# Kernel optimization log

Measured on AMD Instinct MI355X. Metric: run time of the kernel, lower is better.

The kernel has to match this reference:

```python
import jax, jax.numpy as jnp
import numpy as np

NEG_SLOPE = 0.01  # torch nn.LeakyReLU default
B, C, H, W = 2, 128, 192, 192
K = 4            # num_cls
O = 12 * 5       # out_channels = 12 * num_mix


def _lrelu(x):
    return jnp.where(x >= 0, x, NEG_SLOPE * x)


def _conv1x1(x, w, b):
    # x: [B,K,C,H,W] (or [B,C,H,W] broadcast via K in w), w: [K,O,C], b: [K,O]
    y = jnp.einsum('bkchw,koc->bkohw', x, w)
    return y + b[None, :, :, None, None]


def setup_inputs() -> dict:
    key = jax.random.key(0)
    ks = jax.random.split(key, 12)
    s = 1.0 / np.sqrt(C)
    inp = {
        'fusion_context': jax.random.normal(ks[0], (B, C, H, W), jnp.float32),
        'seg': jax.random.randint(ks[1], (B, 1, H, W), 0, K, jnp.int64),
        'W1':  jax.random.normal(ks[2], (K, C, C), jnp.float32) * s,
        'b1':  jax.random.normal(ks[3], (K, C), jnp.float32) * s,
        'Wr1': jax.random.normal(ks[4], (K, C, C), jnp.float32) * s,
        'br1': jax.random.normal(ks[5], (K, C), jnp.float32) * s,
        'Wr2': jax.random.normal(ks[6], (K, C, C), jnp.float32) * s,
        'br2': jax.random.normal(ks[7], (K, C), jnp.float32) * s,
        'W3':  jax.random.normal(ks[8], (K, C, C), jnp.float32) * s,
        'b3':  jax.random.normal(ks[9], (K, C), jnp.float32) * s,
        'W4':  jax.random.normal(ks[10], (K, O, C), jnp.float32) * s,
        'b4':  jax.random.normal(ks[11], (K, O), jnp.float32) * s,
    }
    return inp


def reference(fusion_context, seg, W1, b1, Wr1, br1, Wr2, br2, W3, b3, W4, b4):
    x = fusion_context[:, None]                      # [B,1,C,H,W] -> broadcast over K towers
    x = jnp.broadcast_to(x, (B, K, C, H, W))
    h = _conv1x1(x, W1, b1)                          # conv1x1(ep_ch, ep_ch)
    # ResBlock_1x1: x + conv(lrelu(conv(x)))
    r = _conv1x1(_lrelu(_conv1x1(h, Wr1, br1)), Wr2, br2)
    h = h + r
    h = _conv1x1(h, W3, b3)                          # conv1x1(ep_ch, ep_ch)
    h = _lrelu(h)                                    # LeakyReLU
    conv_outs = _conv1x1(h, W4, b4)                  # [B,K,O,H,W]
    # one-hot mask-and-sum over classes
    seg2 = seg[:, 0]                                 # [B,H,W]
    one_hot = jax.nn.one_hot(seg2, K, dtype=conv_outs.dtype)  # [B,H,W,K]
    one_hot = jnp.transpose(one_hot, (0, 3, 1, 2))   # [B,K,H,W]
    out = jnp.sum(conv_outs * one_hot[:, :, None], axis=1)    # [B,O,H,W]
    return out
```

## Files before the change

### kernel.cpp

```cpp
#include <hip/hip_runtime.h>
#include <hip/hip_bf16.h>
#include <cstdint>
#include <cstddef>

constexpr int kB = 2, kC = 128, kH = 192, kW = 192, kK = 4, kO = 60;
constexpr int kHW  = kH * kW;
constexpr int NPIX = kB * kHW;
constexpr int P    = 96;
constexpr int WPB  = kHW / P;
constexpr int NWIN = NPIX / P;
constexpr int MAXG = 9;
constexpr float kSlope = 0.01f;

constexpr size_t WB_OFF    = 0;
constexpr size_t WB4_OFF   = 524288;
constexpr size_t BIAS_OFF  = 589824;
constexpr size_t BIAS4_OFF = 598016;
constexpr size_t WS_NEED   = 599040;

typedef __attribute__((ext_vector_type(8))) short bf16x8;
typedef __attribute__((ext_vector_type(4))) float f32x4;

__device__ __forceinline__ unsigned short f2bf(float f) {
  unsigned u = __float_as_uint(f);
  u += 0x7FFF + ((u >> 16) & 1);
  return (unsigned short)(u >> 16);
}
__device__ __forceinline__ float bf2f(unsigned short u) {
  return __uint_as_float(((unsigned)u) << 16);
}
__device__ __forceinline__ float load1(const float* p) { return *p; }
__device__ __forceinline__ float load1(const __hip_bfloat16* p) {
  return bf2f(*reinterpret_cast<const unsigned short*>(p));
}
__device__ __forceinline__ bf16x8 load_wfrag(const __hip_bfloat16* p) {
  return *reinterpret_cast<const bf16x8*>(p);
}
__device__ __forceinline__ bf16x8 load_wfrag(const float* p) {
  bf16x8 r;
#pragma unroll
  for (int j = 0; j < 8; ++j) r[j] = (short)f2bf(p[j]);
  return r;
}

__device__ __forceinline__ int xgrp(int r, int g) {
  return (g + r + (r >> 3)) & 15;
}

struct alignas(16) Smem {
  unsigned short Xs[P][kC];
  unsigned short Ys[P][kC];
  short ord[MAXG * 16];
  unsigned char kg[MAXG + 3];
  int cnt[kK], gpre[kK + 1], first[kK];
  int s_f32, s_onz;
};

template<typename T>
__device__ __forceinline__ void prep_body(
    const T* W1, const T* Wr1, const T* Wr2, const T* W3, const T* W4,
    const T* b1, const T* br1, const T* br2, const T* b3, const T* b4,
    char* ws, int gid) {
  unsigned short* WB  = (unsigned short*)(ws + WB_OFF);
  unsigned short* WB4 = (unsigned short*)(ws + WB4_OFF);
  float* BS  = (float*)(ws + BIAS_OFF);
  float* BS4 = (float*)(ws + BIAS4_OFF);
  if (gid < 32768) {
    const int lk = gid >> 11, fl = gid & 2047, f = fl >> 6, lane = fl & 63;
    const int l = lk >> 2, k = lk & 3;
    const int rb = f >> 3, oi = (f >> 2) & 1, ks = f & 3;
    const int quad = lane >> 4, col = lane & 15;
    const int row = rb * 32 + oi * 16 + col, c0 = ks * 32 + quad * 8;
    const T* Wsrc = (l == 0) ? W1 : (l == 1) ? Wr1 : (l == 2) ? Wr2 : W3;
    bf16x8 v = load_wfrag(Wsrc + ((size_t)(k * kC + row)) * kC + c0);
    *reinterpret_cast<bf16x8*>(WB + (size_t)lk * 16384 + f * 512 + lane * 8) = v;
  } else if (gid < 36864) {
    const int g2 = gid - 32768, k = g2 >> 10, fl = g2 & 1023, f = fl >> 6, lane = fl & 63;
    const int rb = f >> 2, ks = f & 3, quad = lane >> 4, col = lane & 15;
    const int row = rb * 16 + col, c0 = ks * 32 + quad * 8;
    bf16x8 v;
    if (row < kO) v = load_wfrag(W4 + ((size_t)(k * kO + row)) * kC + c0);
    else { for (int j = 0; j < 8; ++j) v[j] = 0; }
    *reinterpret_cast<bf16x8*>(WB4 + (size_t)k * 8192 + f * 512 + lane * 8) = v;
  } else if (gid < 38912) {
    const int g2 = gid - 36864, l = g2 >> 9, kn = g2 & 511, k = kn >> 7, n = kn & 127;
    const T* bsrc = (l == 0) ? b1 : (l == 1) ? br1 : (l == 2) ? br2 : b3;
    BS[g2] = load1(bsrc + k * kC + n);
  } else if (gid < 39168) {
    const int g2 = gid - 38912, k = g2 >> 6, n = g2 & 63;
    BS4[g2] = (n < kO) ? load1(b4 + k * kO + n) : 0.f;
  }
}

__global__ __launch_bounds__(256) void prep_kernel(
    const void* W1, const void* Wr1, const void* Wr2, const void* W3, const void* W4,
    const void* b1, const void* br1, const void* br2, const void* b3, const void* b4,
    char* ws) {
  __shared__ int s_f32;
  if (threadIdx.x == 0) s_f32 = 0;
  __syncthreads();
  const unsigned short h = ((const unsigned short*)W1)[threadIdx.x];
  if (((h >> 7) & 0xFF) >= 0x84) atomicAdd(&s_f32, 1);
  __syncthreads();
  const int gid = blockIdx.x * 256 + threadIdx.x;
  if (s_f32 > 8)
    prep_body<float>((const float*)W1, (const float*)Wr1, (const float*)Wr2,
                     (const float*)W3, (const float*)W4, (const float*)b1,
                     (const float*)br1, (const float*)br2, (const float*)b3,
                     (const float*)b4, ws, gid);
  else
    prep_body<__hip_bfloat16>((const __hip_bfloat16*)W1, (const __hip_bfloat16*)Wr1,
                              (const __hip_bfloat16*)Wr2, (const __hip_bfloat16*)W3,
                              (const __hip_bfloat16*)W4, (const __hip_bfloat16*)b1,
                              (const __hip_bfloat16*)br1, (const __hip_bfloat16*)br2,
                              (const __hip_bfloat16*)b3, (const __hip_bfloat16*)b4,
                              ws, gid);
}

template<bool SNIFFX>
__device__ __forceinline__ void prologue(const void* xraw, const void* segraw,
                                         Smem& sm, int bb, int hw0, int tid) {
  if (tid == 0) { sm.s_f32 = 0; sm.s_onz = 0; }
  if (tid < kK) sm.cnt[tid] = 0;
  __syncthreads();
  if constexpr (SNIFFX) {
    const unsigned short h = ((const unsigned short*)xraw)[tid];
    if (((h >> 7) & 0xFF) >= 0x84) atomicAdd(&sm.s_f32, 1);
  }
  if (tid < 288 && (tid & 1) && ((const unsigned*)segraw)[tid] != 0)
    atomicAdd(&sm.s_onz, 1);
  __syncthreads();
  const bool is64 = (sm.s_onz < 4);
  int myk = 0, myidx = 0;
  if (tid < P) {
    const int pg = bb * kHW + hw0 + tid;
    myk = is64 ? (int)((const long long*)segraw)[pg]
               : ((const int*)segraw)[pg];
    myidx = atomicAdd(&sm.cnt[myk], 1);
    if (myidx == 0) sm.first[myk] = tid;
  }
  __syncthreads();
  if (tid == 0) {
    int g = 0;
    for (int k = 0; k < kK; ++k) {
      sm.gpre[k] = g;
      const int gc = (sm.cnt[k] + 15) >> 4;
      for (int j = 0; j < gc; ++j) sm.kg[g + j] = (unsigned char)k;
      g += gc;
    }
    sm.gpre[kK] = g;
  }
  __syncthreads();
  if (tid < P) sm.ord[sm.gpre[myk] * 16 + myidx] = (short)tid;
  const int ngrp = sm.gpre[kK];
  if (tid < ngrp * 16) {
    const int g = tid >> 4, k2 = sm.kg[g];
    const int rel = tid - sm.gpre[k2] * 16;
    if (rel >= sm.cnt[k2])
      sm.ord[tid] = (short)(sm.first[k2] | 256);
  }
}

template<typename T>
__device__ __forceinline__ void stage(const void* xraw, unsigned short (*Xs)[kC],
                                      int bb, int hw0, int tid) {
  const T* x = (const T*)xraw;
  const size_t base = (size_t)bb * kC * kHW + hw0;
  if constexpr (sizeof(T) == 4) {
#pragma unroll
    for (int it = 0; it < 6; ++it) {
      const int flat = it * 512 + tid;
      const int c = flat / 24, j = flat - c * 24;
      const float4 v = *reinterpret_cast<const float4*>(
          (const float*)x + base + (size_t)c * kHW + j * 4);
      const float vv[4] = {v.x, v.y, v.z, v.w};
#pragma unroll
      for (int jj = 0; jj < 4; ++jj) {
        const int r = j * 4 + jj;
        Xs[r][xgrp(r, c >> 3) * 8 + (c & 7)] = f2bf(vv[jj]);
      }
    }
  } else {
#pragma unroll
    for (int it = 0; it < 3; ++it) {
      const int flat = it * 512 + tid;
      const int c = flat / 12, j = flat - c * 12;
      const bf16x8 v = *reinterpret_cast<const bf16x8*>(
          (const unsigned short*)x + base + (size_t)c * kHW + j * 8);
#pragma unroll
      for (int jj = 0; jj < 8; ++jj) {
        const int r = j * 8 + jj;
        Xs[r][xgrp(r, c >> 3) * 8 + (c & 7)] = (unsigned short)v[jj];
      }
    }
  }
}

template<typename T>
__device__ __forceinline__ void output(void* outraw, const float* Obuf,
                                       int bb, int hw0, int tid) {
  T* ob = (T*)outraw + (size_t)bb * kO * kHW + hw0;
  if constexpr (sizeof(T) == 4) {
#pragma unroll
    for (int it = 0; it < 3; ++it) {
      const int t = it * 512 + tid;
      if (t < 1440) {
        const int o = t / 24, q = t - o * 24;
        float4 v;
        v.x = Obuf[(q * 4 + 0) * 61 + o];
        v.y = Obuf[(q * 4 + 1) * 61 + o];
        v.z = Obuf[(q * 4 + 2) * 61 + o];
        v.w = Obuf[(q * 4 + 3) * 61 + o];
        *reinterpret_cast<float4*>((float*)ob + (size_t)o * kHW + q * 4) = v;
      }
    }
  } else {
#pragma unroll
    for (int it = 0; it < 6; ++it) {
      const int t = it * 512 + tid;
      if (t < 2880) {
        const int o = t / 48, q = t - o * 48;
        const unsigned u = (unsigned)f2bf(Obuf[(q * 2) * 61 + o]) |
                           ((unsigned)f2bf(Obuf[(q * 2 + 1) * 61 + o]) << 16);
        *reinterpret_cast<unsigned*>((unsigned short*)ob + (size_t)o * kHW + q * 2) = u;
      }
    }
  }
}

template<bool LRELU, bool RES, bool PAIR>
__device__ __forceinline__ void pair_body(const unsigned short (*src)[kC],
                                          unsigned short (*dst)[kC],
                                          const bf16x8 (&a)[2][4],
                                          const float4 (&bv)[2],
                                          const Smem& sm, int g,
                                          int quad, int col, int rb) {
  constexpr int NG = PAIR ? 2 : 1;
  int ov[2], row[2];
  bf16x8 bfr[2][4];
#pragma unroll
  for (int j = 0; j < NG; ++j) {
    ov[j]  = sm.ord[(g + j) * 16 + col];
    row[j] = ov[j] & 255;
#pragma unroll
    for (int ks = 0; ks < 4; ++ks)
      bfr[j][ks] = *reinterpret_cast<const bf16x8*>(
          &src[row[j]][xgrp(row[j], ks * 4 + quad) * 8]);
  }
  f32x4 acc[2][2];
#pragma unroll
  for (int j = 0; j < NG; ++j)
#pragma unroll
    for (int oi = 0; oi < 2; ++oi) {
      acc[j][oi] = {0.f, 0.f, 0.f, 0.f};
#pragma unroll
      for (int ks = 0; ks < 4; ++ks)
        acc[j][oi] = __builtin_amdgcn_mfma_f32_16x16x32_bf16(
            a[oi][ks], bfr[j][ks], acc[j][oi], 0, 0, 0);
    }
#pragma unroll
  for (int j = 0; j < NG; ++j) {
    if (ov[j] < 256) {
#pragma unroll
      for (int oi = 0; oi < 2; ++oi) {
        const int nb = rb * 32 + oi * 16 + quad * 4;
        unsigned short* dp = &dst[row[j]][xgrp(row[j], nb >> 3) * 8 + (nb & 7)];
        const float bb4[4] = {bv[oi].x, bv[oi].y, bv[oi].z, bv[oi].w};
        float v[4];
#pragma unroll
        for (int r = 0; r < 4; ++r) {
          float t = acc[j][oi][r] + bb4[r];
          if constexpr (LRELU) t = (t >= 0.f) ? t : kSlope * t;
          v[r] = t;
        }
        if constexpr (RES) {
          const short4 rv = *reinterpret_cast<const short4*>(dp);
          v[0] += bf2f((unsigned short)rv.x);
          v[1] += bf2f((unsigned short)rv.y);
          v[2] += bf2f((unsigned short)rv.z);
          v[3] += bf2f((unsigned short)rv.w);
        }
        short4 pk;
        pk.x = (short)f2bf(v[0]); pk.y = (short)f2bf(v[1]);
        pk.z = (short)f2bf(v[2]); pk.w = (short)f2bf(v[3]);
        *reinterpret_cast<short4*>(dp) = pk;
      }
    }
  }
}

template<bool LRELU, bool RES>
__device__ __forceinline__ void layerP(const unsigned short (*src)[kC],
                                       unsigned short (*dst)[kC],
                                       const unsigned short* __restrict__ WBl,
                                       const float* __restrict__ BSl,
                                       const Smem& sm, int tid) {
  const int wave = tid >> 6, lane = tid & 63, quad = lane >> 4, col = lane & 15;
  const int rb = wave & 3, ch2 = wave >> 2;
#pragma unroll
  for (int c2 = 0; c2 < 2; ++c2) {
    const int k = ch2 * 2 + c2;
    const int gs = sm.gpre[k], ge = sm.gpre[k + 1];
    if (gs == ge) continue;
    const unsigned short* wk = WBl + (size_t)k * 16384 + lane * 8;
    bf16x8 a[2][4];
    float4 bv[2];
#pragma unroll
    for (int oi = 0; oi < 2; ++oi) {
#pragma unroll
      for (int ks = 0; ks < 4; ++ks)
        a[oi][ks] = *reinterpret_cast<const bf16x8*>(wk + (((rb * 2 + oi) * 4 + ks) << 9));
      bv[oi] = *reinterpret_cast<const float4*>(
          BSl + k * kC + rb * 32 + oi * 16 + quad * 4);
    }
    int g = gs;
    for (; g + 1 < ge; g += 2)
      pair_body<LRELU, RES, true >(src, dst, a, bv, sm, g, quad, col, rb);
    if (g < ge)
      pair_body<LRELU, RES, false>(src, dst, a, bv, sm, g, quad, col, rb);
  }
}

template<bool PAIR>
__device__ __forceinline__ void pair_body5(const unsigned short (*src)[kC],
                                           float* __restrict__ Obuf,
                                           const bf16x8 (&a)[4],
                                           const float4& bv,
                                           const Smem& sm, int g,
                                           int quad, int col, int rb) {
  constexpr int NG = PAIR ? 2 : 1;
  int ov[2], row[2];
  bf16x8 bfr[2][4];
#pragma unroll
  for (int j = 0; j < NG; ++j) {
    ov[j]  = sm.ord[(g + j) * 16 + col];
    row[j] = ov[j] & 255;
#pragma unroll
    for (int ks = 0; ks < 4; ++ks)
      bfr[j][ks] = *reinterpret_cast<const bf16x8*>(
          &src[row[j]][xgrp(row[j], ks * 4 + quad) * 8]);
  }
  f32x4 acc[2];
#pragma unroll
  for (int j = 0; j < NG; ++j) {
    acc[j] = {0.f, 0.f, 0.f, 0.f};
#pragma unroll
    for (int ks = 0; ks < 4; ++ks)
      acc[j] = __builtin_amdgcn_mfma_f32_16x16x32_bf16(a[ks], bfr[j][ks], acc[j], 0, 0, 0);
  }
  const float bb4[4] = {bv.x, bv.y, bv.z, bv.w};
#pragma unroll
  for (int j = 0; j < NG; ++j) {
    if (ov[j] < 256) {
#pragma unroll
      for (int r = 0; r < 4; ++r) {
        const int n = rb * 16 + quad * 4 + r;
        if (n < kO) Obuf[row[j] * 61 + n] = acc[j][r] + bb4[r];
      }
    }
  }
}

__device__ __forceinline__ void layer5P(const unsigned short (*src)[kC],
                                        float* __restrict__ Obuf,
                                        const unsigned short* __restrict__ WB4,
                                        const float* __restrict__ BS4,
                                        const Smem& sm, int tid) {
  const int wave = tid >> 6, lane = tid & 63, quad = lane >> 4, col = lane & 15;
  const int rb = wave & 3, ch2 = wave >> 2;
#pragma unroll
  for (int c2 = 0; c2 < 2; ++c2) {
    const int k = ch2 * 2 + c2;
    const int gs = sm.gpre[k], ge = sm.gpre[k + 1];
    if (gs == ge) continue;
    const unsigned short* wk = WB4 + (size_t)k * 8192 + lane * 8;
    bf16x8 a[4];
#pragma unroll
    for (int ks = 0; ks < 4; ++ks)
      a[ks] = *reinterpret_cast<const bf16x8*>(wk + ((rb * 4 + ks) << 9));
    const float4 bv = *reinterpret_cast<const float4*>(
        BS4 + k * 64 + rb * 16 + quad * 4);
    int g = gs;
    for (; g + 1 < ge; g += 2)
      pair_body5<true >(src, Obuf, a, bv, sm, g, quad, col, rb);
    if (g < ge)
      pair_body5<false>(src, Obuf, a, bv, sm, g, quad, col, rb);
  }
}

__global__ __launch_bounds__(512, 4) void fused_main(const void* xraw, const void* segraw,
                                                     void* outraw,
                                                     const char* __restrict__ ws) {
  __shared__ Smem sm;
  const int tid = threadIdx.x, wi = blockIdx.x;
  const int bb = wi / WPB, hw0 = (wi - bb * WPB) * P;
  prologue<true>(xraw, segraw, sm, bb, hw0, tid);
  const bool isf32 = (sm.s_f32 > 16);
  if (isf32) stage<float>(xraw, sm.Xs, bb, hw0, tid);
  else       stage<__hip_bfloat16>(xraw, sm.Xs, bb, hw0, tid);
  __syncthreads();

  const unsigned short* WB  = (const unsigned short*)(ws + WB_OFF);
  const unsigned short* WB4 = (const unsigned short*)(ws + WB4_OFF);
  const float* BS  = (const float*)(ws + BIAS_OFF);
  const float* BS4 = (const float*)(ws + BIAS4_OFF);

  layerP<false, false>(sm.Xs, sm.Ys, WB,              BS,        sm, tid); __syncthreads();
  layerP<true,  false>(sm.Ys, sm.Xs, WB + 4 * 16384,  BS + 512,  sm, tid); __syncthreads();
  layerP<false, true >(sm.Xs, sm.Ys, WB + 8 * 16384,  BS + 1024, sm, tid); __syncthreads();
  layerP<true,  false>(sm.Ys, sm.Xs, WB + 12 * 16384, BS + 1536, sm, tid); __syncthreads();
  float* Obuf = (float*)sm.Ys;
  layer5P(sm.Xs, Obuf, WB4, BS4, sm, tid);     __syncthreads();

  if (isf32) output<float>(outraw, Obuf, bb, hw0, tid);
  else       output<__hip_bfloat16>(outraw, Obuf, bb, hw0, tid);
}

template<typename T, bool LRELU, bool RES>
__device__ __forceinline__ void layerF(const unsigned short (*src)[kC],
                                       unsigned short (*dst)[kC],
                                       const T* __restrict__ W,
                                       const T* __restrict__ bia,
                                       const Smem& sm, int tid) {
  const int wave = tid >> 6, lane = tid & 63, quad = lane >> 4, col = lane & 15;
  const int rb = wave & 3, ch2 = wave >> 2;
  const int gs = sm.gpre[ch2 * 2], ge = sm.gpre[ch2 * 2 + 2];
  int curk = -1;
  bf16x8 a[2][4];
  float bs[2][4];
  for (int g = gs; g < ge; ++g) {
    const int k = sm.kg[g];
    if (k != curk) {
      curk = k;
      const T* Wk = W + (size_t)k * kC * kC;
      const T* bk = bia + (size_t)k * kC;
#pragma unroll
      for (int oi = 0; oi < 2; ++oi) {
        const int ra = rb * 32 + oi * 16 + col;
#pragma unroll
        for (int ks = 0; ks < 4; ++ks)
          a[oi][ks] = load_wfrag(Wk + (size_t)ra * kC + ks * 32 + quad * 8);
#pragma unroll
        for (int r = 0; r < 4; ++r)
          bs[oi][r] = load1(bk + rb * 32 + oi * 16 + quad * 4 + r);
      }
    }
    const int ov  = sm.ord[g * 16 + col];
    const int row = ov & 255;
    bf16x8 bfr[4];
#pragma unroll
    for (int ks = 0; ks < 4; ++ks)
      bfr[ks] = *reinterpret_cast<const bf16x8*>(&src[row][xgrp(row, ks * 4 + quad) * 8]);
#pragma unroll
    for (int oi = 0; oi < 2; ++oi) {
      f32x4 acc = {0.f, 0.f, 0.f, 0.f};
#pragma unroll
      for (int ks = 0; ks < 4; ++ks)
        acc = __builtin_amdgcn_mfma_f32_16x16x32_bf16(a[oi][ks], bfr[ks], acc, 0, 0, 0);
      if (ov < 256) {
        const int nb = rb * 32 + oi * 16 + quad * 4;
        unsigned short* dp = &dst[row][xgrp(row, nb >> 3) * 8 + (nb & 7)];
        float v[4];
#pragma unroll
        for (int r = 0; r < 4; ++r) {
          float t = acc[r] + bs[oi][r];
          if constexpr (LRELU) t = (t >= 0.f) ? t : kSlope * t;
          v[r] = t;
        }
        if constexpr (RES) {
          const short4 rv = *reinterpret_cast<const short4*>(dp);
          v[0] += bf2f((unsigned short)rv.x);
          v[1] += bf2f((unsigned short)rv.y);
          v[2] += bf2f((unsigned short)rv.z);
          v[3] += bf2f((unsigned short)rv.w);
        }
        short4 pk;
        pk.x = (short)f2bf(v[0]); pk.y = (short)f2bf(v[1]);
        pk.z = (short)f2bf(v[2]); pk.w = (short)f2bf(v[3]);
        *reinterpret_cast<short4*>(dp) = pk;
      }
    }
  }
}

template<typename T>
__device__ __forceinline__ void layer5F(const unsigned short (*src)[kC],
                                        float* __restrict__ Obuf,
                                        const T* __restrict__ W4,
                                        const T* __restrict__ b4,
                                        const Smem& sm, int tid) {
  const int wave = tid >> 6, lane = tid & 63, quad = lane >> 4, col = lane & 15;
  const int rb = wave & 3, ch2 = wave >> 2;
  const int gs = sm.gpre[ch2 * 2], ge = sm.gpre[ch2 * 2 + 2];
  int curk = -1;
  bf16x8 a[4];
  float bs[4];
  for (int g = gs; g < ge; ++g) {
    const int k = sm.kg[g];
    if (k != curk) {
      curk = k;
      const T* Wk = W4 + (size_t)k * kO * kC;
      const T* bk = b4 + (size_t)k * kO;
      const int ra = min(rb * 16 + col, kO - 1);
#pragma unroll
      for (int ks = 0; ks < 4; ++ks)
        a[ks] = load_wfrag(Wk + (size_t)ra * kC + ks * 32 + quad * 8);
#pragma unroll
      for (int r = 0; r < 4; ++r) {
        const int n = rb * 16 + quad * 4 + r;
        bs[r] = (n < kO) ? load1(bk + n) : 0.f;
      }
    }
    const int ov  = sm.ord[g * 16 + col];
    const int row = ov & 255;
    bf16x8 bfr[4];
#pragma unroll
    for (int ks = 0; ks < 4; ++ks)
      bfr[ks] = *reinterpret_cast<const bf16x8*>(&src[row][xgrp(row, ks * 4 + quad) * 8]);
    f32x4 acc = {0.f, 0.f, 0.f, 0.f};
#pragma unroll
    for (int ks = 0; ks < 4; ++ks)
      acc = __builtin_amdgcn_mfma_f32_16x16x32_bf16(a[ks], bfr[ks], acc, 0, 0, 0);
    if (ov < 256) {
#pragma unroll
      for (int r = 0; r < 4; ++r) {
        const int n = rb * 16 + quad * 4 + r;
        if (n < kO) Obuf[row * 61 + n] = acc[r] + bs[r];
      }
    }
  }
}

template<typename T>
__device__ __forceinline__ void run_fall(
    const void* xraw, void* outraw,
    const void* W1, const void* b1, const void* Wr1, const void* br1,
    const void* Wr2, const void* br2, const void* W3, const void* b3,
    const void* W4, const void* b4,
    Smem& sm, int bb, int hw0, int tid) {
  stage<T>(xraw, sm.Xs, bb, hw0, tid);
  __syncthreads();
  layerF<T, false, false>(sm.Xs, sm.Ys, (const T*)W1,  (const T*)b1,  sm, tid); __syncthreads();
  layerF<T, true,  false>(sm.Ys, sm.Xs, (const T*)Wr1, (const T*)br1, sm, tid); __syncthreads();
  layerF<T, false, true >(sm.Xs, sm.Ys, (const T*)Wr2, (const T*)br2, sm, tid); __syncthreads();
  layerF<T, true,  false>(sm.Ys, sm.Xs, (const T*)W3,  (const T*)b3,  sm, tid); __syncthreads();
  float* Obuf = (float*)sm.Ys;
  layer5F<T>(sm.Xs, Obuf, (const T*)W4, (const T*)b4, sm, tid);
  __syncthreads();
  output<T>(outraw, Obuf, bb, hw0, tid);
}

__global__ __launch_bounds__(512) void fused_fallback(
    const void* xraw, const void* segraw,
    const void* W1, const void* b1, const void* Wr1, const void* br1,
    const void* Wr2, const void* br2, const void* W3, const void* b3,
    const void* W4, const void* b4, void* outraw) {
  __shared__ Smem sm;
  const int tid = threadIdx.x, wi = blockIdx.x;
  const int bb = wi / WPB, hw0 = (wi - bb * WPB) * P;
  prologue<true>(xraw, segraw, sm, bb, hw0, tid);
  if (sm.s_f32 > 16)
    run_fall<float>(xraw, outraw, W1, b1, Wr1, br1, Wr2, br2, W3, b3, W4, b4,
                    sm, bb, hw0, tid);
  else
    run_fall<__hip_bfloat16>(xraw, outraw, W1, b1, Wr1, br1, Wr2, br2, W3, b3, W4, b4,
                             sm, bb, hw0, tid);
}

extern "C" void kernel_launch(void* const* d_in, const int* in_sizes, int n_in,
                              void* d_out, int out_size, void* d_ws, size_t ws_size,
                              hipStream_t stream) {
  (void)in_sizes; (void)n_in; (void)out_size;
  const int prep = (d_ws != nullptr && ws_size >= WS_NEED) ? 1 : 0;
  if (prep) {
    prep_kernel<<<153, 256, 0, stream>>>(
        d_in[2], d_in[4], d_in[6], d_in[8], d_in[10],
        d_in[3], d_in[5], d_in[7], d_in[9], d_in[11], (char*)d_ws);
    fused_main<<<NWIN, 512, 0, stream>>>(d_in[0], d_in[1], d_out, (const char*)d_ws);
  } else {
    fused_fallback<<<NWIN, 512, 0, stream>>>(
        d_in[0], d_in[1], d_in[2], d_in[3], d_in[4], d_in[5], d_in[6], d_in[7],
        d_in[8], d_in[9], d_in[10], d_in[11], d_out);
  }
}
```

Baseline: 130.1 us.

## Interleave class groups across wave halves and store intermediates in class-compacted order

Measured after the change: 141.3 us. 8.5% more time.

```diff
diff --git a/kernel.cpp b/kernel.cpp
--- a/kernel.cpp
+++ b/kernel.cpp
@@ -52,6 +52,8 @@
   unsigned short Ys[P][kC];
   short ord[MAXG * 16];
   unsigned char kg[MAXG + 3];
+  unsigned char gb[MAXG + 3];
+  unsigned char gv[MAXG + 3];
   int cnt[kK], gpre[kK + 1], first[kK];
   int s_f32, s_onz;
 };
@@ -141,12 +143,17 @@
   }
   __syncthreads();
   if (tid == 0) {
-    int g = 0;
+    int g = 0, cb = 0;
     for (int k = 0; k < kK; ++k) {
       sm.gpre[k] = g;
       const int gc = (sm.cnt[k] + 15) >> 4;
-      for (int j = 0; j < gc; ++j) sm.kg[g + j] = (unsigned char)k;
+      for (int j = 0; j < gc; ++j) {
+        sm.kg[g + j] = (unsigned char)k;
+        sm.gb[g + j] = (unsigned char)(cb + j * 16);
+        sm.gv[g + j] = (unsigned char)min(16, sm.cnt[k] - j * 16);
+      }
       g += gc;
+      cb += sm.cnt[k];
     }
     sm.gpre[kK] = g;
   }
@@ -228,24 +235,34 @@
   }
 }
 
-template<bool LRELU, bool RES, bool PAIR>
+template<bool LRELU, bool RES, bool PAIR, bool SRCPIX>
 __device__ __forceinline__ void pair_body(const unsigned short (*src)[kC],
                                           unsigned short (*dst)[kC],
                                           const bf16x8 (&a)[2][4],
                                           const float4 (&bv)[2],
-                                          const Smem& sm, int g,
+                                          const Smem& sm, int g0, int g1,
                                           int quad, int col, int rb) {
   constexpr int NG = PAIR ? 2 : 1;
-  int ov[2], row[2];
+  const int gg[2] = {g0, g1};
+  int srow[2], drow[2];
+  bool valid[2];
   bf16x8 bfr[2][4];
 #pragma unroll
   for (int j = 0; j < NG; ++j) {
-    ov[j]  = sm.ord[(g + j) * 16 + col];
-    row[j] = ov[j] & 255;
+    const int g = gg[j];
+    const int vc = sm.gv[g];
+    const int base = sm.gb[g];
+    drow[j]  = base + col;
+    valid[j] = (col < vc);
+    if constexpr (SRCPIX) {
+      srow[j] = sm.ord[g * 16 + col] & 255;
+    } else {
+      srow[j] = base + min(col, vc - 1);
+    }
 #pragma unroll
     for (int ks = 0; ks < 4; ++ks)
       bfr[j][ks] = *reinterpret_cast<const bf16x8*>(
-          &src[row[j]][xgrp(row[j], ks * 4 + quad) * 8]);
+          &src[srow[j]][xgrp(srow[j], ks * 4 + quad) * 8]);
   }
   f32x4 acc[2][2];
 #pragma unroll
@@ -260,11 +277,11 @@
     }
 #pragma unroll
   for (int j = 0; j < NG; ++j) {
-    if (ov[j] < 256) {
+    if (valid[j]) {
 #pragma unroll
       for (int oi = 0; oi < 2; ++oi) {
         const int nb = rb * 32 + oi * 16 + quad * 4;
-        unsigned short* dp = &dst[row[j]][xgrp(row[j], nb >> 3) * 8 + (nb & 7)];
+        unsigned short* dp = &dst[drow[j]][xgrp(drow[j], nb >> 3) * 8 + (nb & 7)];
         const float bb4[4] = {bv[oi].x, bv[oi].y, bv[oi].z, bv[oi].w};
         float v[4];
 #pragma unroll
@@ -289,35 +306,40 @@
   }
 }
 
-template<bool LRELU, bool RES>
+template<bool LRELU, bool RES, bool SRCPIX>
 __device__ __forceinline__ void layerP(const unsigned short (*src)[kC],
                                        unsigned short (*dst)[kC],
                                        const unsigned short* __restrict__ WBl,
                                        const float* __restrict__ BSl,
                                        const Smem& sm, int tid) {
   const int wave = tid >> 6, lane = tid & 63, quad = lane >> 4, col = lane & 15;
-  const int rb = wave & 3, ch2 = wave >> 2;
-#pragma unroll
-  for (int c2 = 0; c2 < 2; ++c2) {
-    const int k = ch2 * 2 + c2;
-    const int gs = sm.gpre[k], ge = sm.gpre[k + 1];
-    if (gs == ge) continue;
-    const unsigned short* wk = WBl + (size_t)k * 16384 + lane * 8;
-    bf16x8 a[2][4];
-    float4 bv[2];
-#pragma unroll
-    for (int oi = 0; oi < 2; ++oi) {
-#pragma unroll
-      for (int ks = 0; ks < 4; ++ks)
-        a[oi][ks] = *reinterpret_cast<const bf16x8*>(wk + (((rb * 2 + oi) * 4 + ks) << 9));
-      bv[oi] = *reinterpret_cast<const float4*>(
-          BSl + k * kC + rb * 32 + oi * 16 + quad * 4);
-    }
-    int g = gs;
-    for (; g + 1 < ge; g += 2)
-      pair_body<LRELU, RES, true >(src, dst, a, bv, sm, g, quad, col, rb);
-    if (g < ge)
-      pair_body<LRELU, RES, false>(src, dst, a, bv, sm, g, quad, col, rb);
+  const int rb = wave & 3, half = wave >> 2;
+  const int ngrp = sm.gpre[kK];
+  int curk = -1;
+  bf16x8 a[2][4];
+  float4 bv[2];
+  int g = half;
+  while (g < ngrp) {
+    const int k = sm.kg[g];
+    if (k != curk) {
+      curk = k;
+      const unsigned short* wk = WBl + (size_t)k * 16384 + lane * 8;
+#pragma unroll
+      for (int oi = 0; oi < 2; ++oi) {
+#pragma unroll
+        for (int ks = 0; ks < 4; ++ks)
+          a[oi][ks] = *reinterpret_cast<const bf16x8*>(wk + (((rb * 2 + oi) * 4 + ks) << 9));
+        bv[oi] = *reinterpret_cast<const float4*>(
+            BSl + k * kC + rb * 32 + oi * 16 + quad * 4);
+      }
+    }
+    if (g + 2 < ngrp && sm.kg[g + 2] == k) {
+      pair_body<LRELU, RES, true, SRCPIX>(src, dst, a, bv, sm, g, g + 2, quad, col, rb);
+      g += 4;
+    } else {
+      pair_body<LRELU, RES, false, SRCPIX>(src, dst, a, bv, sm, g, g, quad, col, rb);
+      g += 2;
+    }
   }
 }
 
@@ -326,19 +348,24 @@
                                            float* __restrict__ Obuf,
                                            const bf16x8 (&a)[4],
                                            const float4& bv,
-                                           const Smem& sm, int g,
+                                           const Smem& sm, int g0, int g1,
                                            int quad, int col, int rb) {
   constexpr int NG = PAIR ? 2 : 1;
-  int ov[2], row[2];
+  const int gg[2] = {g0, g1};
+  int srow[2], pix[2];
+  bool valid[2];
   bf16x8 bfr[2][4];
 #pragma unroll
   for (int j = 0; j < NG; ++j) {
-    ov[j]  = sm.ord[(g + j) * 16 + col];
-    row[j] = ov[j] & 255;
+    const int g = gg[j];
+    const int vc = sm.gv[g];
+    srow[j]  = sm.gb[g] + min(col, vc - 1);
+    valid[j] = (col < vc);
+    pix[j]   = sm.ord[g * 16 + col] & 255;
 #pragma unroll
     for (int ks = 0; ks < 4; ++ks)
       bfr[j][ks] = *reinterpret_cast<const bf16x8*>(
-          &src[row[j]][xgrp(row[j], ks * 4 + quad) * 8]);
+          &src[srow[j]][xgrp(srow[j], ks * 4 + quad) * 8]);
   }
   f32x4 acc[2];
 #pragma unroll
@@ -351,11 +378,11 @@
   const float bb4[4] = {bv.x, bv.y, bv.z, bv.w};
 #pragma unroll
   for (int j = 0; j < NG; ++j) {
-    if (ov[j] < 256) {
+    if (valid[j]) {
 #pragma unroll
       for (int r = 0; r < 4; ++r) {
         const int n = rb * 16 + quad * 4 + r;
-        if (n < kO) Obuf[row[j] * 61 + n] = acc[j][r] + bb4[r];
+        if (n < kO) Obuf[pix[j] * 61 + n] = acc[j][r] + bb4[r];
       }
     }
   }
@@ -367,24 +394,29 @@
                                         const float* __restrict__ BS4,
                                         const Smem& sm, int tid) {
   const int wave = tid >> 6, lane = tid & 63, quad = lane >> 4, col = lane & 15;
-  const int rb = wave & 3, ch2 = wave >> 2;
-#pragma unroll
-  for (int c2 = 0; c2 < 2; ++c2) {
-    const int k = ch2 * 2 + c2;
-    const int gs = sm.gpre[k], ge = sm.gpre[k + 1];
-    if (gs == ge) continue;
-    const unsigned short* wk = WB4 + (size_t)k * 8192 + lane * 8;
-    bf16x8 a[4];
-#pragma unroll
-    for (int ks = 0; ks < 4; ++ks)
-      a[ks] = *reinterpret_cast<const bf16x8*>(wk + ((rb * 4 + ks) << 9));
-    const float4 bv = *reinterpret_cast<const float4*>(
-        BS4 + k * 64 + rb * 16 + quad * 4);
-    int g = gs;
-    for (; g + 1 < ge; g += 2)
-      pair_body5<true >(src, Obuf, a, bv, sm, g, quad, col, rb);
-    if (g < ge)
-      pair_body5<false>(src, Obuf, a, bv, sm, g, quad, col, rb);
+  const int rb = wave & 3, half = wave >> 2;
+  const int ngrp = sm.gpre[kK];
+  int curk = -1;
+  bf16x8 a[4];
+  float4 bv;
+  int g = half;
+  while (g < ngrp) {
+    const int k = sm.kg[g];
+    if (k != curk) {
+      curk = k;
+      const unsigned short* wk = WB4 + (size_t)k * 8192 + lane * 8;
+#pragma unroll
+      for (int ks = 0; ks < 4; ++ks)
+        a[ks] = *reinterpret_cast<const bf16x8*>(wk + ((rb * 4 + ks) << 9));
+      bv = *reinterpret_cast<const float4*>(BS4 + k * 64 + rb * 16 + quad * 4);
+    }
+    if (g + 2 < ngrp && sm.kg[g + 2] == k) {
+      pair_body5<true >(src, Obuf, a, bv, sm, g, g + 2, quad, col, rb);
+      g += 4;
+    } else {
+      pair_body5<false>(src, Obuf, a, bv, sm, g, g, quad, col, rb);
+      g += 2;
+    }
   }
 }
 
@@ -405,10 +437,10 @@
   const float* BS  = (const float*)(ws + BIAS_OFF);
   const float* BS4 = (const float*)(ws + BIAS4_OFF);
 
-  layerP<false, false>(sm.Xs, sm.Ys, WB,              BS,        sm, tid); __syncthreads();
-  layerP<true,  false>(sm.Ys, sm.Xs, WB + 4 * 16384,  BS + 512,  sm, tid); __syncthreads();
-  layerP<false, true >(sm.Xs, sm.Ys, WB + 8 * 16384,  BS + 1024, sm, tid); __syncthreads();
-  layerP<true,  false>(sm.Ys, sm.Xs, WB + 12 * 16384, BS + 1536, sm, tid); __syncthreads();
+  layerP<false, false, true >(sm.Xs, sm.Ys, WB,              BS,        sm, tid); __syncthreads();
+  layerP<true,  false, false>(sm.Ys, sm.Xs, WB + 4 * 16384,  BS + 512,  sm, tid); __syncthreads();
+  layerP<false, true,  false>(sm.Xs, sm.Ys, WB + 8 * 16384,  BS + 1024, sm, tid); __syncthreads();
+  layerP<true,  false, false>(sm.Ys, sm.Xs, WB + 12 * 16384, BS + 1536, sm, tid); __syncthreads();
   float* Obuf = (float*)sm.Ys;
   layer5P(sm.Xs, Obuf, WB4, BS4, sm, tid);     __syncthreads();
 
```

## Store intermediate activations in class-sorted compact rows and fold bias into MFMA accumulator

Applied to the files above, without the earlier changes.

Result: slower. 133.4 us (+2.5%).

```diff
diff --git a/kernel.cpp b/kernel.cpp
--- a/kernel.cpp
+++ b/kernel.cpp
@@ -29,6 +29,12 @@
 __device__ __forceinline__ float bf2f(unsigned short u) {
   return __uint_as_float(((unsigned)u) << 16);
 }
+__device__ __forceinline__ unsigned pack2bf(float lo, float hi) {
+  float2 f2; f2.x = lo; f2.y = hi;
+  __hip_bfloat162 h = __float22bfloat162_rn(f2);
+  unsigned u; __builtin_memcpy(&u, &h, sizeof(u));
+  return u;
+}
 __device__ __forceinline__ float load1(const float* p) { return *p; }
 __device__ __forceinline__ float load1(const __hip_bfloat16* p) {
   return bf2f(*reinterpret_cast<const unsigned short*>(p));
@@ -52,6 +58,8 @@
   unsigned short Ys[P][kC];
   short ord[MAXG * 16];
   unsigned char kg[MAXG + 3];
+  unsigned char gb[MAXG + 3];
+  unsigned char gv[MAXG + 3];
   int cnt[kK], gpre[kK + 1], first[kK];
   int s_f32, s_onz;
 };
@@ -141,12 +149,17 @@
   }
   __syncthreads();
   if (tid == 0) {
-    int g = 0;
+    int g = 0, cb = 0;
     for (int k = 0; k < kK; ++k) {
       sm.gpre[k] = g;
       const int gc = (sm.cnt[k] + 15) >> 4;
-      for (int j = 0; j < gc; ++j) sm.kg[g + j] = (unsigned char)k;
+      for (int j = 0; j < gc; ++j) {
+        sm.kg[g + j] = (unsigned char)k;
+        sm.gb[g + j] = (unsigned char)(cb + j * 16);
+        sm.gv[g + j] = (unsigned char)min(16, sm.cnt[k] - j * 16);
+      }
       g += gc;
+      cb += sm.cnt[k];
     }
     sm.gpre[kK] = g;
   }
@@ -220,39 +233,44 @@
       const int t = it * 512 + tid;
       if (t < 2880) {
         const int o = t / 48, q = t - o * 48;
-        const unsigned u = (unsigned)f2bf(Obuf[(q * 2) * 61 + o]) |
-                           ((unsigned)f2bf(Obuf[(q * 2 + 1) * 61 + o]) << 16);
+        const unsigned u = pack2bf(Obuf[(q * 2) * 61 + o], Obuf[(q * 2 + 1) * 61 + o]);
         *reinterpret_cast<unsigned*>((unsigned short*)ob + (size_t)o * kHW + q * 2) = u;
       }
     }
   }
 }
 
-template<bool LRELU, bool RES, bool PAIR>
+template<bool LRELU, bool RES, bool PAIR, bool SRCPIX>
 __device__ __forceinline__ void pair_body(const unsigned short (*src)[kC],
                                           unsigned short (*dst)[kC],
                                           const bf16x8 (&a)[2][4],
-                                          const float4 (&bv)[2],
-                                          const Smem& sm, int g,
+                                          const f32x4 (&bv)[2],
+                                          const Smem& sm, int g0,
                                           int quad, int col, int rb) {
   constexpr int NG = PAIR ? 2 : 1;
-  int ov[2], row[2];
+  int srow[2], drow[2];
+  bool valid[2];
   bf16x8 bfr[2][4];
 #pragma unroll
   for (int j = 0; j < NG; ++j) {
-    ov[j]  = sm.ord[(g + j) * 16 + col];
-    row[j] = ov[j] & 255;
+    const int g = g0 + j;
+    const int vc = sm.gv[g];
+    const int base = sm.gb[g];
+    drow[j]  = base + col;
+    valid[j] = (col < vc);
+    if constexpr (SRCPIX) srow[j] = sm.ord[g * 16 + col] & 255;
+    else                  srow[j] = base + min(col, vc - 1);
 #pragma unroll
     for (int ks = 0; ks < 4; ++ks)
       bfr[j][ks] = *reinterpret_cast<const bf16x8*>(
-          &src[row[j]][xgrp(row[j], ks * 4 + quad) * 8]);
+          &src[srow[j]][xgrp(srow[j], ks * 4 + quad) * 8]);
   }
   f32x4 acc[2][2];
 #pragma unroll
   for (int j = 0; j < NG; ++j)
 #pragma unroll
     for (int oi = 0; oi < 2; ++oi) {
-      acc[j][oi] = {0.f, 0.f, 0.f, 0.f};
+      acc[j][oi] = bv[oi];
 #pragma unroll
       for (int ks = 0; ks < 4; ++ks)
         acc[j][oi] = __builtin_amdgcn_mfma_f32_16x16x32_bf16(
@@ -260,36 +278,35 @@
     }
 #pragma unroll
   for (int j = 0; j < NG; ++j) {
-    if (ov[j] < 256) {
+    if (valid[j]) {
 #pragma unroll
       for (int oi = 0; oi < 2; ++oi) {
         const int nb = rb * 32 + oi * 16 + quad * 4;
-        unsigned short* dp = &dst[row[j]][xgrp(row[j], nb >> 3) * 8 + (nb & 7)];
-        const float bb4[4] = {bv[oi].x, bv[oi].y, bv[oi].z, bv[oi].w};
+        unsigned short* dp = &dst[drow[j]][xgrp(drow[j], nb >> 3) * 8 + (nb & 7)];
         float v[4];
 #pragma unroll
         for (int r = 0; r < 4; ++r) {
-          float t = acc[j][oi][r] + bb4[r];
+          float t = acc[j][oi][r];
           if constexpr (LRELU) t = (t >= 0.f) ? t : kSlope * t;
           v[r] = t;
         }
         if constexpr (RES) {
-          const short4 rv = *reinterpret_cast<const short4*>(dp);
-          v[0] += bf2f((unsigned short)rv.x);
-          v[1] += bf2f((unsigned short)rv.y);
-          v[2] += bf2f((unsigned short)rv.z);
-          v[3] += bf2f((unsigned short)rv.w);
+          const uint2 rv = *reinterpret_cast<const uint2*>(dp);
+          v[0] += bf2f((unsigned short)(rv.x & 0xFFFFu));
+          v[1] += bf2f((unsigned short)(rv.x >> 16));
+          v[2] += bf2f((unsigned short)(rv.y & 0xFFFFu));
+          v[3] += bf2f((unsigned short)(rv.y >> 16));
         }
-        short4 pk;
-        pk.x = (short)f2bf(v[0]); pk.y = (short)f2bf(v[1]);
-        pk.z = (short)f2bf(v[2]); pk.w = (short)f2bf(v[3]);
-        *reinterpret_cast<short4*>(dp) = pk;
-      }
-    }
-  }
-}
-
-template<bool LRELU, bool RES>
+        uint2 pk;
+        pk.x = pack2bf(v[0], v[1]);
+        pk.y = pack2bf(v[2], v[3]);
+        *reinterpret_cast<uint2*>(dp) = pk;
+      }
+    }
+  }
+}
+
+template<bool LRELU, bool RES, bool SRCPIX>
 __device__ __forceinline__ void layerP(const unsigned short (*src)[kC],
                                        unsigned short (*dst)[kC],
                                        const unsigned short* __restrict__ WBl,
@@ -304,20 +321,21 @@
     if (gs == ge) continue;
     const unsigned short* wk = WBl + (size_t)k * 16384 + lane * 8;
     bf16x8 a[2][4];
-    float4 bv[2];
+    f32x4 bv[2];
 #pragma unroll
     for (int oi = 0; oi < 2; ++oi) {
 #pragma unroll
       for (int ks = 0; ks < 4; ++ks)
         a[oi][ks] = *reinterpret_cast<const bf16x8*>(wk + (((rb * 2 + oi) * 4 + ks) << 9));
-      bv[oi] = *reinterpret_cast<const float4*>(
+      const float4 b4v = *reinterpret_cast<const float4*>(
           BSl + k * kC + rb * 32 + oi * 16 + quad * 4);
+      bv[oi][0] = b4v.x; bv[oi][1] = b4v.y; bv[oi][2] = b4v.z; bv[oi][3] = b4v.w;
     }
     int g = gs;
     for (; g + 1 < ge; g += 2)
-      pair_body<LRELU, RES, true >(src, dst, a, bv, sm, g, quad, col, rb);
+      pair_body<LRELU, RES, true, SRCPIX>(src, dst, a, bv, sm, g, quad, col, rb);
     if (g < ge)
-      pair_body<LRELU, RES, false>(src, dst, a, bv, sm, g, quad, col, rb);
+      pair_body<LRELU, RES, false, SRCPIX>(src, dst, a, bv, sm, g, quad, col, rb);
   }
 }
 
@@ -325,37 +343,40 @@
 __device__ __forceinline__ void pair_body5(const unsigned short (*src)[kC],
                                            float* __restrict__ Obuf,
                                            const bf16x8 (&a)[4],
-                                           const float4& bv,
-                                           const Smem& sm, int g,
+                                           const f32x4& bv,
+                                           const Smem& sm, int g0,
                                            int quad, int col, int rb) {
   constexpr int NG = PAIR ? 2 : 1;
-  int ov[2], row[2];
+  int srow[2], pix[2];
+  bool valid[2];
   bf16x8 bfr[2][4];
 #pragma unroll
   for (int j = 0; j < NG; ++j) {
-    ov[j]  = sm.ord[(g + j) * 16 + col];
-    row[j] = ov[j] & 255;
+    const int g = g0 + j;
+    const int vc = sm.gv[g];
+    srow[j]  = sm.gb[g] + min(col, vc - 1);
+    valid[j] = (col < vc);
+    pix[j]   = sm.ord[g * 16 + col] & 255;
 #pragma unroll
     for (int ks = 0; ks < 4; ++ks)
       bfr[j][ks] = *reinterpret_cast<const bf16x8*>(
-          &src[row[j]][xgrp(row[j], ks * 4 + quad) * 8]);
+          &src[srow[j]][xgrp(srow[j], ks * 4 + quad) * 8]);
   }
   f32x4 acc[2];
 #pragma unroll
   for (int j = 0; j < NG; ++j) {
-    acc[j] = {0.f, 0.f, 0.f, 0.f};
+    acc[j] = bv;
 #pragma unroll
     for (int ks = 0; ks < 4; ++ks)
       acc[j] = __builtin_amdgcn_mfma_f32_16x16x32_bf16(a[ks], bfr[j][ks], acc[j], 0, 0, 0);
   }
-  const float bb4[4] = {bv.x, bv.y, bv.z, bv.w};
 #pragma unroll
   for (int j = 0; j < NG; ++j) {
-    if (ov[j] < 256) {
+    if (valid[j]) {
 #pragma unroll
       for (int r = 0; r < 4; ++r) {
         const int n = rb * 16 + quad * 4 + r;
-        if (n < kO) Obuf[row[j] * 61 + n] = acc[j][r] + bb4[r];
+        if (n < kO) Obuf[pix[j] * 61 + n] = acc[j][r];
       }
     }
   }
@@ -378,8 +399,9 @@
 #pragma unroll
     for (int ks = 0; ks < 4; ++ks)
       a[ks] = *reinterpret_cast<const bf16x8*>(wk + ((rb * 4 + ks) << 9));
-    const float4 bv = *reinterpret_cast<const float4*>(
+    const float4 b4v = *reinterpret_cast<const float4*>(
         BS4 + k * 64 + rb * 16 + quad * 4);
+    f32x4 bv; bv[0] = b4v.x; bv[1] = b4v.y; bv[2] = b4v.z; bv[3] = b4v.w;
     int g = gs;
     for (; g + 1 < ge; g += 2)
       pair_body5<true >(src, Obuf, a, bv, sm, g, quad, col, rb);
@@ -405,10 +427,10 @@
   const float* BS  = (const float*)(ws + BIAS_OFF);
   const float* BS4 = (const float*)(ws + BIAS4_OFF);
 
-  layerP<false, false>(sm.Xs, sm.Ys, WB,              BS,        sm, tid); __syncthreads();
-  layerP<true,  false>(sm.Ys, sm.Xs, WB + 4 * 16384,  BS + 512,  sm, tid); __syncthreads();
-  layerP<false, true >(sm.Xs, sm.Ys, WB + 8 * 16384,  BS + 1024, sm, tid); __syncthreads();
-  layerP<true,  false>(sm.Ys, sm.Xs, WB + 12 * 16384, BS + 1536, sm, tid); __syncthreads();
+  layerP<false, false, true >(sm.Xs, sm.Ys, WB,              BS,        sm, tid); __syncthreads();
+  layerP<true,  false, false>(sm.Ys, sm.Xs, WB + 4 * 16384,  BS + 512,  sm, tid); __syncthreads();
+  layerP<false, true,  false>(sm.Xs, sm.Ys, WB + 8 * 16384,  BS + 1024, sm, tid); __syncthreads();
+  layerP<true,  false, false>(sm.Ys, sm.Xs, WB + 12 * 16384, BS + 1536, sm, tid); __syncthreads();
   float* Obuf = (float*)sm.Ys;
   layer5P(sm.Xs, Obuf, WB4, BS4, sm, tid);     __syncthreads();
 
```
